# Optimization experiments

Hardware: AMD Instinct MI355X
Metric: run time of the kernel (lower is better)

## Reference

```python
import jax, jax.numpy as jnp
import numpy as np

TOP_K = 2


def setup_inputs() -> dict:
    key = jax.random.key(0)
    k1, k2, k3, k4, k5 = jax.random.split(key, 5)
    H, F, E = 1024, 2048, 8
    B, S = 2, 1024
    return {
        "hidden_states": jax.random.normal(k1, (B, S, H), dtype=jnp.float32),
        "gate_w": jax.random.normal(k2, (E, H), dtype=jnp.float32) * (1.0 / np.sqrt(H)),
        "w1": jax.random.normal(k3, (E, F, H), dtype=jnp.float32) * (1.0 / np.sqrt(H)),
        "w2": jax.random.normal(k4, (E, H, F), dtype=jnp.float32) * (1.0 / np.sqrt(F)),
        "w3": jax.random.normal(k5, (E, F, H), dtype=jnp.float32) * (1.0 / np.sqrt(H)),
    }


def reference(hidden_states, gate_w, w1, w2, w3):
    B, S, H = hidden_states.shape
    E = gate_w.shape[0]
    x = hidden_states.reshape(-1, H)  # [T, H]

    # Router: softmax in float32, top-k, renormalize (exact Mixtral math)
    router_logits = x @ gate_w.T  # [T, E]
    probs = jax.nn.softmax(router_logits.astype(jnp.float32), axis=-1)
    routing_weights, selected = jax.lax.top_k(probs, TOP_K)  # [T, K]
    routing_weights = routing_weights / routing_weights.sum(axis=-1, keepdims=True)
    routing_weights = routing_weights.astype(x.dtype)

    # Per-token combine weight for each expert: [T, E]
    combine = (jax.nn.one_hot(selected, E, dtype=x.dtype) * routing_weights[..., None]).sum(axis=1)

    # Dense grouped expert SwiGLU MLP (zero combine weight for unselected experts
    # makes this strictly equivalent to the gathered/dispatched computation)
    h = jnp.einsum('th,efh->etf', x, w1)   # [E, T, F]
    g = jnp.einsum('th,efh->etf', x, w3)   # [E, T, F]
    mid = jax.nn.silu(h) * g               # SwiGLU
    expert_out = jnp.einsum('etf,ehf->eth', mid, w2)  # [E, T, H]
    out = jnp.einsum('eth,te->th', expert_out, combine)  # weighted combine

    return out.reshape(B, S, H), router_logits
```

## Files before the change

kernel.cpp:

```cpp
#include <hip/hip_runtime.h>
#include <hip/hip_bf16.h>
#include <math.h>

#define H 1024
#define FF 2048
#define E 8
#define T 2048
#define NSLOT (2*T)
#define SLOT_PAD 128

#define WCONV_BLKS 24576
#define XCONV_BLKS 1024
#define ROUTER_BLKS T
#define K1_BLKS (WCONV_BLKS + XCONV_BLKS + ROUTER_BLKS)

typedef __attribute__((ext_vector_type(8))) short s16x8;
typedef __attribute__((ext_vector_type(4))) float f32x4;
typedef __attribute__((ext_vector_type(4))) unsigned int u32x4;

static __device__ __forceinline__ unsigned short f2bf(float f) {
    union { float f; unsigned u; } v; v.f = f;
    unsigned r = v.u + 0x7fff + ((v.u >> 16) & 1);
    return (unsigned short)(r >> 16);
}
static __device__ __forceinline__ float bf2f(unsigned short s) {
    union { unsigned u; float f; } v; v.u = ((unsigned)s) << 16;
    return v.f;
}
static __device__ __forceinline__ unsigned pack2(float a, float b) {
    return (unsigned)f2bf(a) | ((unsigned)f2bf(b) << 16);
}

typedef __attribute__((address_space(3))) unsigned int lds_uint;
typedef const __attribute__((address_space(1))) unsigned int glob_uint;
static __device__ __forceinline__ void gl_lds16(const void* g, void* l) {
    __builtin_amdgcn_global_load_lds((glob_uint*)g, (lds_uint*)l, 16, 0, 0);
}

static __device__ __forceinline__ void expert_range(const int* __restrict__ counts,
                                                    int e, int& off, int& cnt) {
    int acc = 0;
    #pragma unroll
    for (int i = 0; i < E; ++i) {
        int c = counts[i];
        if (i < e) acc += c;
        if (i == e) cnt = c;
    }
    off = acc;
}

__global__ __launch_bounds__(256) void prep_kernel(
    const float* __restrict__ x, const float* __restrict__ gw,
    const float* __restrict__ w1, const float* __restrict__ w3,
    const float* __restrict__ w2,
    unsigned short* __restrict__ w1b, unsigned short* __restrict__ w3b,
    unsigned short* __restrict__ w2b, unsigned short* __restrict__ xb,
    float* __restrict__ logits_out, int* __restrict__ top_id,
    float* __restrict__ top_w, int* __restrict__ counts)
{
    int b = blockIdx.x;
    int tid = threadIdx.x;
    if (b < WCONV_BLKS + XCONV_BLKS) {
        const float* s; unsigned short* d; size_t i;
        if (b < WCONV_BLKS) {
            int r = b >> 13;
            s = (r == 0) ? w1 : (r == 1) ? w3 : w2;
            d = (r == 0) ? w1b : (r == 1) ? w3b : w2b;
            i = ((size_t)(b & 8191) * 256 + tid) * 8;
        } else {
            s = x; d = xb;
            i = ((size_t)(b - WCONV_BLKS) * 256 + tid) * 8;
        }
        f32x4 a0 = *(const f32x4*)(s + i);
        f32x4 a1 = *(const f32x4*)(s + i + 4);
        u32x4 r0;
        r0.x = pack2(a0.x, a0.y); r0.y = pack2(a0.z, a0.w);
        r0.z = pack2(a1.x, a1.y); r0.w = pack2(a1.z, a1.w);
        *(u32x4*)(d + i) = r0;
        return;
    }
    int t = b - (WCONV_BLKS + XCONV_BLKS);
    int e = tid >> 5;
    int l32 = tid & 31;
    const float* xr = x + (size_t)t * H;
    const float* gr = gw + (size_t)e * H;
    float s = 0.f;
    for (int h = l32; h < H; h += 32) s += xr[h] * gr[h];
    for (int off = 16; off; off >>= 1) s += __shfl_down(s, off, 32);
    __shared__ float lg[E];
    if (l32 == 0) lg[e] = s;
    __syncthreads();
    if (tid < E) logits_out[(size_t)t * E + tid] = lg[tid];
    if (tid == 0) {
        int i1 = 0; float b1 = lg[0];
        for (int i = 1; i < E; ++i) if (lg[i] > b1) { b1 = lg[i]; i1 = i; }
        int i2 = -1; float b2 = -INFINITY;
        for (int i = 0; i < E; ++i) if (i != i1 && lg[i] > b2) { b2 = lg[i]; i2 = i; }
        float p2 = expf(b2 - b1);
        float inv = 1.f / (1.f + p2);
        top_id[2*t]   = i1;  top_id[2*t+1] = i2;
        top_w[2*t]    = inv; top_w[2*t+1]  = p2 * inv;
        atomicAdd(&counts[i1], 1);
        atomicAdd(&counts[i2], 1);
    }
}

__global__ __launch_bounds__(256) void assign_kernel(
    const int* __restrict__ top_id, const int* __restrict__ counts,
    int* __restrict__ cursors, int* __restrict__ top_pos,
    int* __restrict__ slot_token)
{
    int t = blockIdx.x * 256 + threadIdx.x;
    if (t >= T) return;
    int offs[E];
    {
        int acc = 0;
        #pragma unroll
        for (int i = 0; i < E; ++i) { offs[i] = acc; acc += counts[i]; }
    }
    #pragma unroll
    for (int k = 0; k < 2; ++k) {
        int e = top_id[2*t + k];
        int p = offs[e] + atomicAdd(&cursors[e], 1);
        top_pos[2*t + k] = p;
        slot_token[p] = t;
    }
}

__global__ __launch_bounds__(256) void gemm1_kernel(
    const unsigned short* __restrict__ xb, const int* __restrict__ slot_token,
    const unsigned short* __restrict__ w1b, const unsigned short* __restrict__ w3b,
    const int* __restrict__ counts, unsigned short* __restrict__ mid)
{
    int e = blockIdx.z;
    int off, cnt;
    expert_range(counts, e, off, cnt);
    int m0 = blockIdx.y * 128;
    if (m0 >= cnt) return;
    int f0 = blockIdx.x * 64;

    __shared__ __align__(16) unsigned short sx[128 * 64];
    __shared__ __align__(16) unsigned short sb[128 * 64];

    int tid = threadIdx.x;
    int wv = tid >> 6, ln = tid & 63;
    int quad = ln >> 4, l16 = ln & 15;
    int wm = wv & 1, wn = wv >> 1;
    int xor7 = l16 & 7;

    const unsigned short* xsrc[4]; unsigned short* xdst[4];
    #pragma unroll
    for (int j = 0; j < 4; ++j) {
        int row = wv * 32 + j * 8 + (ln >> 3);
        int slot = off + m0 + row;
        if (m0 + row >= cnt) slot = off;
        int tok = slot_token[slot];
        int cl = (ln & 7) ^ (row & 7);
        xsrc[j] = xb + (size_t)tok * H + cl * 8;
        xdst[j] = &sx[(wv * 32 + j * 8) * 64];
    }
    const unsigned short* bsrc[4]; unsigned short* bdst[4];
    #pragma unroll
    for (int j = 0; j < 4; ++j) {
        int row = wv * 32 + j * 8 + (ln >> 3);
        const unsigned short* wsel = (row & 1) ? w3b : w1b;
        int f = f0 + (row >> 1);
        int cl = (ln & 7) ^ (row & 7);
        bsrc[j] = wsel + ((size_t)e * FF + f) * H + cl * 8;
        bdst[j] = &sb[(wv * 32 + j * 8) * 64];
    }

    f32x4 acc[4][4];
    #pragma unroll
    for (int i = 0; i < 4; ++i)
        #pragma unroll
        for (int j = 0; j < 4; ++j) acc[i][j] = (f32x4){0.f, 0.f, 0.f, 0.f};

    for (int k0 = 0; k0 < H; k0 += 64) {
        #pragma unroll
        for (int j = 0; j < 4; ++j) gl_lds16(xsrc[j] + k0, xdst[j]);
        #pragma unroll
        for (int j = 0; j < 4; ++j) gl_lds16(bsrc[j] + k0, bdst[j]);
        __syncthreads();
        #pragma unroll
        for (int ks = 0; ks < 2; ++ks) {
            int cph = ((quad + 4 * ks) ^ xor7) << 3;
            s16x8 a[4], b[4];
            #pragma unroll
            for (int i = 0; i < 4; ++i)
                a[i] = *(const s16x8*)&sx[(wm * 64 + i * 16 + l16) * 64 + cph];
            #pragma unroll
            for (int j = 0; j < 4; ++j)
                b[j] = *(const s16x8*)&sb[(wn * 64 + j * 16 + l16) * 64 + cph];
            #pragma unroll
            for (int i = 0; i < 4; ++i)
                #pragma unroll
                for (int j = 0; j < 4; ++j)
                    acc[i][j] = __builtin_amdgcn_mfma_f32_16x16x32_bf16(a[i], b[j], acc[i][j], 0, 0, 0);
        }
        __syncthreads();
    }

    bool evenlane = (l16 & 1) == 0;
    #pragma unroll
    for (int i = 0; i < 4; ++i) {
        #pragma unroll
        for (int r = 0; r < 4; ++r) {
            int row = wm * 64 + i * 16 + quad * 4 + r;
            bool live = (m0 + row < cnt);
            size_t base = (size_t)(off + m0 + row) * FF + f0 + wn * 32;
            #pragma unroll
            for (int j = 0; j < 4; ++j) {
                float hv = acc[i][j][r];
                float gv = __shfl_xor(hv, 1);
                if (live && evenlane) {
                    float v = hv / (1.f + __expf(-hv)) * gv;
                    mid[base + j * 8 + (l16 >> 1)] = f2bf(v);
                }
            }
        }
    }
}

__global__ __launch_bounds__(256) void gemm2_kernel(
    const unsigned short* __restrict__ mid, const unsigned short* __restrict__ w2b,
    const int* __restrict__ counts, unsigned short* __restrict__ y)
{
    int e = blockIdx.z;
    int off, cnt;
    expert_range(counts, e, off, cnt);
    int m0 = blockIdx.y * 128;
    if (m0 >= cnt) return;
    int n0 = blockIdx.x * 64;

    __shared__ __align__(16) unsigned short sa[128 * 64];
    __shared__ __align__(16) unsigned short sb[64 * 64];

    int tid = threadIdx.x;
    int wv = tid >> 6, ln = tid & 63;
    int quad = ln >> 4, l16 = ln & 15;
    int wm = wv & 1, wn = wv >> 1;
    int xor7 = l16 & 7;

    const unsigned short* asrc[4]; unsigned short* adst[4];
    #pragma unroll
    for (int j = 0; j < 4; ++j) {
        int row = wv * 32 + j * 8 + (ln >> 3);
        int cl = (ln & 7) ^ (row & 7);
        asrc[j] = mid + (size_t)(off + m0 + row) * FF + cl * 8;
        adst[j] = &sa[(wv * 32 + j * 8) * 64];
    }
    const unsigned short* bsrc[2]; unsigned short* bdst[2];
    #pragma unroll
    for (int j = 0; j < 2; ++j) {
        int row = wv * 16 + j * 8 + (ln >> 3);
        int cl = (ln & 7) ^ (row & 7);
        bsrc[j] = w2b + ((size_t)e * H + n0 + row) * FF + cl * 8;
        bdst[j] = &sb[(wv * 16 + j * 8) * 64];
    }

    f32x4 acc[4][2];
    #pragma unroll
    for (int i = 0; i < 4; ++i)
        #pragma unroll
        for (int j = 0; j < 2; ++j) acc[i][j] = (f32x4){0.f, 0.f, 0.f, 0.f};

    for (int k0 = 0; k0 < FF; k0 += 64) {
        #pragma unroll
        for (int j = 0; j < 4; ++j) gl_lds16(asrc[j] + k0, adst[j]);
        #pragma unroll
        for (int j = 0; j < 2; ++j) gl_lds16(bsrc[j] + k0, bdst[j]);
        __syncthreads();
        #pragma unroll
        for (int ks = 0; ks < 2; ++ks) {
            int cph = ((quad + 4 * ks) ^ xor7) << 3;
            s16x8 a[4], b[2];
            #pragma unroll
            for (int i = 0; i < 4; ++i)
                a[i] = *(const s16x8*)&sa[(wm * 64 + i * 16 + l16) * 64 + cph];
            #pragma unroll
            for (int j = 0; j < 2; ++j)
                b[j] = *(const s16x8*)&sb[(wn * 32 + j * 16 + l16) * 64 + cph];
            #pragma unroll
            for (int i = 0; i < 4; ++i)
                #pragma unroll
                for (int j = 0; j < 2; ++j)
                    acc[i][j] = __builtin_amdgcn_mfma_f32_16x16x32_bf16(a[i], b[j], acc[i][j], 0, 0, 0);
        }
        __syncthreads();
    }

    #pragma unroll
    for (int i = 0; i < 4; ++i) {
        #pragma unroll
        for (int r = 0; r < 4; ++r) {
            int row = wm * 64 + i * 16 + quad * 4 + r;
            if (m0 + row < cnt) {
                size_t base = (size_t)(off + m0 + row) * H + n0 + wn * 32;
                #pragma unroll
                for (int j = 0; j < 2; ++j)
                    y[base + j * 16 + l16] = f2bf(acc[i][j][r]);
            }
        }
    }
}

__global__ __launch_bounds__(256) void combine_kernel(
    const unsigned short* __restrict__ y, const int* __restrict__ top_pos,
    const float* __restrict__ top_w, float* __restrict__ out)
{
    int t = blockIdx.x, tid = threadIdx.x;
    int p0 = top_pos[2*t], p1 = top_pos[2*t+1];
    float w0 = top_w[2*t], w1 = top_w[2*t+1];
    ushort4 a = ((const ushort4*)(y + (size_t)p0 * H))[tid];
    ushort4 b = ((const ushort4*)(y + (size_t)p1 * H))[tid];
    float4 o;
    o.x = w0 * bf2f(a.x) + w1 * bf2f(b.x);
    o.y = w0 * bf2f(a.y) + w1 * bf2f(b.y);
    o.z = w0 * bf2f(a.z) + w1 * bf2f(b.z);
    o.w = w0 * bf2f(a.w) + w1 * bf2f(b.w);
    ((float4*)(out + (size_t)t * H))[tid] = o;
}

extern "C" void kernel_launch(void* const* d_in, const int* in_sizes, int n_in,
                              void* d_out, int out_size, void* d_ws, size_t ws_size,
                              hipStream_t stream) {
    const float* x  = (const float*)d_in[0];
    const float* gw = (const float*)d_in[1];
    const float* w1 = (const float*)d_in[2];
    const float* w2 = (const float*)d_in[3];
    const float* w3 = (const float*)d_in[4];
    float* out    = (float*)d_out;
    float* logits = out + (size_t)T * H;

    int* counts      = (int*)d_ws;
    int* cursors     = counts + 8;
    int* top_id      = counts + 16;
    int* top_pos     = top_id + 2*T;
    int* slot_token  = top_pos + 2*T;
    float* top_w     = (float*)(slot_token + NSLOT);
    unsigned short* xb  = (unsigned short*)(top_w + 2*T);
    unsigned short* mid = xb  + (size_t)T * H;
    unsigned short* y   = mid + (size_t)(NSLOT + SLOT_PAD) * FF;
    unsigned short* w1b = y   + (size_t)NSLOT * H;
    unsigned short* w3b = w1b + (size_t)E * FF * H;
    unsigned short* w2b = w3b + (size_t)E * FF * H;

    (void)hipMemsetAsync(counts, 0, 16 * sizeof(int), stream);

    prep_kernel<<<K1_BLKS, 256, 0, stream>>>(x, gw, w1, w3, w2,
                                             w1b, w3b, w2b, xb,
                                             logits, top_id, top_w, counts);
    assign_kernel<<<(T + 255) / 256, 256, 0, stream>>>(top_id, counts, cursors,
                                                       top_pos, slot_token);
    gemm1_kernel<<<dim3(FF / 64, 16, E), 256, 0, stream>>>(xb, slot_token,
                                                           w1b, w3b, counts, mid);
    gemm2_kernel<<<dim3(H / 64, 16, E), 256, 0, stream>>>(mid, w2b, counts, y);
    combine_kernel<<<T, 256, 0, stream>>>(y, top_pos, top_w, out);
}
```

Baseline: 423.5 us.

## Fuse fp32-to-bf16 weight conversion into GEMM tile loads

The separate pass in the prep kernel that converted w1, w3 and w2 to bf16 is removed. The two GEMM kernels now read fp32 weight tiles directly, pack them to bf16 in registers and store them to LDS, while the activation tiles still use direct global-to-LDS loads. This removes a large standalone read/write pass over all the weights. In exchange, each weight tile is fetched at twice the byte width by every live token block, and the async LDS load for B is replaced by a synchronous register round trip, which may expose more latency.

```diff
diff --git a/kernel.cpp b/kernel.cpp
--- a/kernel.cpp
+++ b/kernel.cpp
@@ -9,10 +9,9 @@
 #define NSLOT (2*T)
 #define SLOT_PAD 128
 
-#define WCONV_BLKS 24576
+#define ROUTER_BLKS T
 #define XCONV_BLKS 1024
-#define ROUTER_BLKS T
-#define K1_BLKS (WCONV_BLKS + XCONV_BLKS + ROUTER_BLKS)
+#define K1_BLKS (ROUTER_BLKS + XCONV_BLKS)
 
 typedef __attribute__((ext_vector_type(8))) short s16x8;
 typedef __attribute__((ext_vector_type(4))) float f32x4;
@@ -51,35 +50,23 @@
 
 __global__ __launch_bounds__(256) void prep_kernel(
     const float* __restrict__ x, const float* __restrict__ gw,
-    const float* __restrict__ w1, const float* __restrict__ w3,
-    const float* __restrict__ w2,
-    unsigned short* __restrict__ w1b, unsigned short* __restrict__ w3b,
-    unsigned short* __restrict__ w2b, unsigned short* __restrict__ xb,
+    unsigned short* __restrict__ xb,
     float* __restrict__ logits_out, int* __restrict__ top_id,
     float* __restrict__ top_w, int* __restrict__ counts)
 {
     int b = blockIdx.x;
     int tid = threadIdx.x;
-    if (b < WCONV_BLKS + XCONV_BLKS) {
-        const float* s; unsigned short* d; size_t i;
-        if (b < WCONV_BLKS) {
-            int r = b >> 13;
-            s = (r == 0) ? w1 : (r == 1) ? w3 : w2;
-            d = (r == 0) ? w1b : (r == 1) ? w3b : w2b;
-            i = ((size_t)(b & 8191) * 256 + tid) * 8;
-        } else {
-            s = x; d = xb;
-            i = ((size_t)(b - WCONV_BLKS) * 256 + tid) * 8;
-        }
-        f32x4 a0 = *(const f32x4*)(s + i);
-        f32x4 a1 = *(const f32x4*)(s + i + 4);
+    if (b >= ROUTER_BLKS) {
+        size_t i = ((size_t)(b - ROUTER_BLKS) * 256 + tid) * 8;
+        f32x4 a0 = *(const f32x4*)(x + i);
+        f32x4 a1 = *(const f32x4*)(x + i + 4);
         u32x4 r0;
         r0.x = pack2(a0.x, a0.y); r0.y = pack2(a0.z, a0.w);
         r0.z = pack2(a1.x, a1.y); r0.w = pack2(a1.z, a1.w);
-        *(u32x4*)(d + i) = r0;
+        *(u32x4*)(xb + i) = r0;
         return;
     }
-    int t = b - (WCONV_BLKS + XCONV_BLKS);
+    int t = b;
     int e = tid >> 5;
     int l32 = tid & 31;
     const float* xr = x + (size_t)t * H;
@@ -129,7 +116,7 @@
 
 __global__ __launch_bounds__(256) void gemm1_kernel(
     const unsigned short* __restrict__ xb, const int* __restrict__ slot_token,
-    const unsigned short* __restrict__ w1b, const unsigned short* __restrict__ w3b,
+    const float* __restrict__ w1, const float* __restrict__ w3,
     const int* __restrict__ counts, unsigned short* __restrict__ mid)
 {
     int e = blockIdx.z;
@@ -159,15 +146,15 @@
         xsrc[j] = xb + (size_t)tok * H + cl * 8;
         xdst[j] = &sx[(wv * 32 + j * 8) * 64];
     }
-    const unsigned short* bsrc[4]; unsigned short* bdst[4];
+    const float* bsrc[4]; unsigned short* bdst[4];
     #pragma unroll
     for (int j = 0; j < 4; ++j) {
         int row = wv * 32 + j * 8 + (ln >> 3);
-        const unsigned short* wsel = (row & 1) ? w3b : w1b;
+        const float* wsel = (row & 1) ? w3 : w1;
         int f = f0 + (row >> 1);
         int cl = (ln & 7) ^ (row & 7);
         bsrc[j] = wsel + ((size_t)e * FF + f) * H + cl * 8;
-        bdst[j] = &sb[(wv * 32 + j * 8) * 64];
+        bdst[j] = &sb[(wv * 32 + j * 8) * 64 + ln * 8];
     }
 
     f32x4 acc[4][4];
@@ -179,8 +166,19 @@
     for (int k0 = 0; k0 < H; k0 += 64) {
         #pragma unroll
         for (int j = 0; j < 4; ++j) gl_lds16(xsrc[j] + k0, xdst[j]);
-        #pragma unroll
-        for (int j = 0; j < 4; ++j) gl_lds16(bsrc[j] + k0, bdst[j]);
+        f32x4 b0[4], b1[4];
+        #pragma unroll
+        for (int j = 0; j < 4; ++j) {
+            b0[j] = *(const f32x4*)(bsrc[j] + k0);
+            b1[j] = *(const f32x4*)(bsrc[j] + k0 + 4);
+        }
+        #pragma unroll
+        for (int j = 0; j < 4; ++j) {
+            u32x4 p;
+            p.x = pack2(b0[j].x, b0[j].y); p.y = pack2(b0[j].z, b0[j].w);
+            p.z = pack2(b1[j].x, b1[j].y); p.w = pack2(b1[j].z, b1[j].w);
+            *(u32x4*)bdst[j] = p;
+        }
         __syncthreads();
         #pragma unroll
         for (int ks = 0; ks < 2; ++ks) {
@@ -223,7 +221,7 @@
 }
 
 __global__ __launch_bounds__(256) void gemm2_kernel(
-    const unsigned short* __restrict__ mid, const unsigned short* __restrict__ w2b,
+    const unsigned short* __restrict__ mid, const float* __restrict__ w2,
     const int* __restrict__ counts, unsigned short* __restrict__ y)
 {
     int e = blockIdx.z;
@@ -250,13 +248,13 @@
         asrc[j] = mid + (size_t)(off + m0 + row) * FF + cl * 8;
         adst[j] = &sa[(wv * 32 + j * 8) * 64];
     }
-    const unsigned short* bsrc[2]; unsigned short* bdst[2];
+    const float* bsrc[2]; unsigned short* bdst[2];
     #pragma unroll
     for (int j = 0; j < 2; ++j) {
         int row = wv * 16 + j * 8 + (ln >> 3);
         int cl = (ln & 7) ^ (row & 7);
-        bsrc[j] = w2b + ((size_t)e * H + n0 + row) * FF + cl * 8;
-        bdst[j] = &sb[(wv * 16 + j * 8) * 64];
+        bsrc[j] = w2 + ((size_t)e * H + n0 + row) * FF + cl * 8;
+        bdst[j] = &sb[(wv * 16 + j * 8) * 64 + ln * 8];
     }
 
     f32x4 acc[4][2];
@@ -268,8 +266,19 @@
     for (int k0 = 0; k0 < FF; k0 += 64) {
         #pragma unroll
         for (int j = 0; j < 4; ++j) gl_lds16(asrc[j] + k0, adst[j]);
-        #pragma unroll
-        for (int j = 0; j < 2; ++j) gl_lds16(bsrc[j] + k0, bdst[j]);
+        f32x4 b0[2], b1[2];
+        #pragma unroll
+        for (int j = 0; j < 2; ++j) {
+            b0[j] = *(const f32x4*)(bsrc[j] + k0);
+            b1[j] = *(const f32x4*)(bsrc[j] + k0 + 4);
+        }
+        #pragma unroll
+        for (int j = 0; j < 2; ++j) {
+            u32x4 p;
+            p.x = pack2(b0[j].x, b0[j].y); p.y = pack2(b0[j].z, b0[j].w);
+            p.z = pack2(b1[j].x, b1[j].y); p.w = pack2(b1[j].z, b1[j].w);
+            *(u32x4*)bdst[j] = p;
+        }
         __syncthreads();
         #pragma unroll
         for (int ks = 0; ks < 2; ++ks) {
@@ -342,19 +351,14 @@
     unsigned short* xb  = (unsigned short*)(top_w + 2*T);
     unsigned short* mid = xb  + (size_t)T * H;
     unsigned short* y   = mid + (size_t)(NSLOT + SLOT_PAD) * FF;
-    unsigned short* w1b = y   + (size_t)NSLOT * H;
-    unsigned short* w3b = w1b + (size_t)E * FF * H;
-    unsigned short* w2b = w3b + (size_t)E * FF * H;
 
     (void)hipMemsetAsync(counts, 0, 16 * sizeof(int), stream);
 
-    prep_kernel<<<K1_BLKS, 256, 0, stream>>>(x, gw, w1, w3, w2,
-                                             w1b, w3b, w2b, xb,
-                                             logits, top_id, top_w, counts);
+    prep_kernel<<<K1_BLKS, 256, 0, stream>>>(x, gw, xb, logits, top_id, top_w, counts);
     assign_kernel<<<(T + 255) / 256, 256, 0, stream>>>(top_id, counts, cursors,
                                                        top_pos, slot_token);
     gemm1_kernel<<<dim3(FF / 64, 16, E), 256, 0, stream>>>(xb, slot_token,
-                                                           w1b, w3b, counts, mid);
-    gemm2_kernel<<<dim3(H / 64, 16, E), 256, 0, stream>>>(mid, w2b, counts, y);
+                                                           w1, w3, counts, mid);
+    gemm2_kernel<<<dim3(H / 64, 16, E), 256, 0, stream>>>(mid, w2, counts, y);
     combine_kernel<<<T, 256, 0, stream>>>(y, top_pos, top_w, out);
 }
```

After: 427.1 us. No clear change (+0.8%).
